# Performance work log

Hardware: AMD Instinct MI355X
Metric: run time of the kernel (lower is better)

Reference implementation:

```python
import jax, jax.numpy as jnp
import numpy as np

NCLASS = 8
THRESH = 0.02
POOL_KS = (32, 16, 8)  # ceil(0.5*64), ceil(0.5*32), ceil(0.5*16)
BN_EPS = 1e-5


def _gcn(x, m, W, b):
    A = m + jnp.eye(x.shape[1], dtype=x.dtype)
    dinv = jax.lax.rsqrt(A.sum(-1))
    An = dinv[:, :, None] * A * dinv[:, None, :]
    return jnp.einsum('bij,bjf->bif', An, x @ W) + b


def _sagpool(x, m, w1, w2, b, k):
    # SAGPooling with GraphConv scorer: s = x w1 + (A x) w2 + b; top-k, gate by tanh
    s = (x @ w1 + jnp.einsum('bij,bjf->bif', m, x) @ w2 + b)[..., 0]
    v, idx = jax.lax.top_k(s, k)
    xg = jnp.take_along_axis(x, idx[:, :, None], axis=1) * jnp.tanh(v)[:, :, None]
    mg = jnp.take_along_axis(jnp.take_along_axis(m, idx[:, :, None], 1), idx[:, None, :], 2)
    return xg, mg


def _readout(x):
    return jnp.concatenate([x.max(1), x.mean(1)], axis=-1)  # [gmp || gep]


def _edist(a, b):
    d2 = (a * a).sum(-1)[:, None] + (b * b).sum(-1)[None, :] - 2.0 * (a @ b.T)
    return jnp.sqrt(jnp.clip(d2, 1e-12))


def _conv1d(x, W, b, dil, pad):
    y = jax.lax.conv_general_dilated(x, W, (1,), [(pad, pad)], rhs_dilation=(dil,),
                                     dimension_numbers=('NCH', 'OIH', 'NCH'))
    return jax.nn.relu(y + b[None, :, None])


def _forward(x, labels, idx_train, gat_W, gat_a1, gat_a2, gcn1_W, gcn1_b, gcn2_W, gcn2_b,
             gcn3_W, gcn3_b, pool1_w1, pool1_w2, pool1_b, pool2_w1, pool2_w2, pool2_b,
             pool3_w1, pool3_w2, pool3_b, gru_Wih, gru_Whh, gru_bih, gru_bhh,
             conv1_W, conv1_b, conv2_W, conv2_b, conv3_W, conv3_b,
             fc0_W, fc0_b, bn0_g, bn0_b, fc1_W, fc1_b, att_W1, att_b1, att_W2, att_b2):
    B, C, L = x.shape
    # GAT-style learned adjacency over the C channel-nodes, thresholded to a sparse graph
    h = x @ gat_W
    e = jax.nn.leaky_relu((h @ gat_a1)[:, :, None] + (h @ gat_a2)[:, None, :], 0.2)
    A = jax.nn.softmax(e, axis=-1)
    m = (A > THRESH).astype(x.dtype)  # [B,C,C] block-diagonal-equivalent mask
    # three GCN + SAGPool stages with summed jump-knowledge readout
    g = jax.nn.relu(_gcn(x, m, gcn1_W, gcn1_b))
    g, m = _sagpool(g, m, pool1_w1, pool1_w2, pool1_b, POOL_KS[0])
    r = _readout(g)
    g = jax.nn.relu(_gcn(g, m, gcn2_W, gcn2_b))
    g, m = _sagpool(g, m, pool2_w1, pool2_w2, pool2_b, POOL_KS[1])
    r = r + _readout(g)
    g = jax.nn.relu(_gcn(g, m, gcn3_W, gcn3_b))
    g, m = _sagpool(g, m, pool3_w1, pool3_w2, pool3_b, POOL_KS[2])
    x_gnn = r + _readout(g)  # [B, 2*hidden]
    # GRU: torch nn.GRU(len_ts, gru_dim) with [N,C,L] -> seq axis 0, batch axis 1 (as in source)
    G = gru_Whh.shape[1]
    def step(hprev, xt):
        gi = xt @ gru_Wih.T + gru_bih
        gh = hprev @ gru_Whh.T + gru_bhh
        ir, iz, inn = jnp.split(gi, 3, axis=-1)
        hr, hz, hn = jnp.split(gh, 3, axis=-1)
        rg = jax.nn.sigmoid(ir + hr)
        zg = jax.nn.sigmoid(iz + hz)
        ng = jnp.tanh(inn + rg * hn)
        hnew = (1.0 - zg) * ng + zg * hprev
        return hnew, hnew
    _, ys = jax.lax.scan(step, jnp.zeros((C, G), x.dtype), x)
    x_gru = ys.mean(1)  # [B, G]
    # dilated conv branch; padding = dilation*(kernel-1) both sides as in __init__
    xc = _conv1d(x, conv1_W, conv1_b, 1, 7)
    xc = _conv1d(xc, conv2_W, conv2_b, 2, 8)
    xc = _conv1d(xc, conv3_W, conv3_b, 4, 8)
    x_conv = xc.mean(2)  # [B, filters[2]]
    feat = jnp.concatenate([x_conv, x_gru, x_gnn], axis=1)
    # mapping MLP: Linear -> BatchNorm(train stats) -> LeakyReLU -> Linear
    hm = feat @ fc0_W + fc0_b
    hm = bn0_g * (hm - hm.mean(0)) * jax.lax.rsqrt(hm.var(0) + BN_EPS) + bn0_b
    hm = jax.nn.leaky_relu(hm, 0.01)
    z = hm @ fc1_W + fc1_b  # [B, 128]
    # per-class attention-weighted prototypes over training samples (masked softmax)
    train = jnp.zeros((B,), bool).at[idx_train].set(True)
    cmask = train[None, :] & (labels[None, :] == jnp.arange(NCLASS)[:, None])
    t = jnp.tanh(jnp.einsum('nd,cda->cna', z, att_W1) + att_b1[:, None, :])
    logits = jnp.einsum('cna,ca->cn', t, att_W2) + att_b2[:, None]
    w = jax.nn.softmax(jnp.where(cmask, logits, -1e30), axis=1)
    proto = w @ z  # [NCLASS, 128]
    pd = jnp.exp(-0.5 * _edist(proto, proto))
    proto_dist = pd.sum() / (NCLASS * (NCLASS - 1) / 2)
    dists = jnp.exp(-0.5 * _edist(z, proto))
    return dists, proto_dist


def setup_inputs() -> dict:
    key = jax.random.key(0)
    ks = iter(jax.random.split(key, 64))
    def rn(shape, s=0.05):
        return jax.random.normal(next(ks), shape, jnp.float32) * s
    B, C, L, H, G, NC, AT, F1 = 256, 64, 512, 128, 128, 8, 64, 128
    inp = {}
    inp['x'] = jax.random.normal(next(ks), (B, C, L), jnp.float32)
    inp['labels'] = jnp.arange(B, dtype=jnp.int32) % NC  # guarantees every class in train split
    inp['idx_train'] = jnp.arange(B // 2, dtype=jnp.int32)
    inp['gat_W'] = rn((L, L)); inp['gat_a1'] = rn((L,)); inp['gat_a2'] = rn((L,))
    inp['gcn1_W'] = rn((L, H)); inp['gcn1_b'] = jnp.zeros((H,), jnp.float32)
    inp['gcn2_W'] = rn((H, H)); inp['gcn2_b'] = jnp.zeros((H,), jnp.float32)
    inp['gcn3_W'] = rn((H, H)); inp['gcn3_b'] = jnp.zeros((H,), jnp.float32)
    for i in (1, 2, 3):
        inp['pool%d_w1' % i] = rn((H, 1)); inp['pool%d_w2' % i] = rn((H, 1))
        inp['pool%d_b' % i] = jnp.zeros((1,), jnp.float32)
    inp['gru_Wih'] = rn((3 * G, L)); inp['gru_Whh'] = rn((3 * G, G))
    inp['gru_bih'] = jnp.zeros((3 * G,), jnp.float32); inp['gru_bhh'] = jnp.zeros((3 * G,), jnp.float32)
    inp['conv1_W'] = rn((F1, C, 8)); inp['conv1_b'] = jnp.zeros((F1,), jnp.float32)
    inp['conv2_W'] = rn((F1, F1, 5)); inp['conv2_b'] = jnp.zeros((F1,), jnp.float32)
    inp['conv3_W'] = rn((F1, F1, 3)); inp['conv3_b'] = jnp.zeros((F1,), jnp.float32)
    inp['fc0_W'] = rn((F1 + G + 2 * H, 256)); inp['fc0_b'] = jnp.zeros((256,), jnp.float32)
    inp['bn0_g'] = jnp.ones((256,), jnp.float32); inp['bn0_b'] = jnp.zeros((256,), jnp.float32)
    inp['fc1_W'] = rn((256, 128)); inp['fc1_b'] = jnp.zeros((128,), jnp.float32)
    inp['att_W1'] = rn((NC, 128, AT)); inp['att_b1'] = jnp.zeros((NC, AT), jnp.float32)
    inp['att_W2'] = rn((NC, AT)); inp['att_b2'] = jnp.zeros((NC,), jnp.float32)
    return inp


def reference(x, labels, idx_train, gat_W, gat_a1, gat_a2, gcn1_W, gcn1_b, gcn2_W, gcn2_b,
              gcn3_W, gcn3_b, pool1_w1, pool1_w2, pool1_b, pool2_w1, pool2_w2, pool2_b,
              pool3_w1, pool3_w2, pool3_b, gru_Wih, gru_Whh, gru_bih, gru_bhh,
              conv1_W, conv1_b, conv2_W, conv2_b, conv3_W, conv3_b,
              fc0_W, fc0_b, bn0_g, bn0_b, fc1_W, fc1_b, att_W1, att_b1, att_W2, att_b2):
    return _forward(x, labels, idx_train, gat_W, gat_a1, gat_a2, gcn1_W, gcn1_b, gcn2_W, gcn2_b,
                    gcn3_W, gcn3_b, pool1_w1, pool1_w2, pool1_b, pool2_w1, pool2_w2, pool2_b,
                    pool3_w1, pool3_w2, pool3_b, gru_Wih, gru_Whh, gru_bih, gru_bhh,
                    conv1_W, conv1_b, conv2_W, conv2_b, conv3_W, conv3_b,
                    fc0_W, fc0_b, bn0_g, bn0_b, fc1_W, fc1_b, att_W1, att_b1, att_W2, att_b2)
```

## Files before the change

kernel.cpp:

```cpp
#include <hip/hip_runtime.h>
#include <math.h>

#define BB 256
#define CC 64
#define LL 512
#define HH 128
#define G3 384
#define NC 8
#define AT 64
#define CL1 519
#define CL2 527
#define CL3 535
#define THRESH 0.02f

typedef _Float16 h2 __attribute__((ext_vector_type(2)));
typedef _Float16 f16x8 __attribute__((ext_vector_type(8)));
typedef float f32x4 __attribute__((ext_vector_type(4)));
union HU { unsigned int u; h2 h; float f; };
union BU { uint4 u; f16x8 h; };

__device__ inline float warp_red_sum(float v) {
  #pragma unroll
  for (int o = 32; o > 0; o >>= 1) v += __shfl_down(v, o, 64);
  return v;
}

__device__ inline float fdot2f(h2 a, h2 b, float c) {
#if __has_builtin(__builtin_amdgcn_fdot2)
  return __builtin_amdgcn_fdot2(a, b, c, false);
#else
  float r;
  asm volatile("v_dot2_f32_f16 %0, %1, %2, %3" : "=v"(r) : "v"(a), "v"(b), "v"(c));
  return r;
#endif
}
__device__ inline h2 asH2(float f) { HU u; u.f = f; return u.h; }
__device__ inline h2 uH2(unsigned int x) { HU u; u.u = x; return u.h; }
__device__ inline unsigned int packh(float a, float b) {
  HU u; h2 t; t.x = (_Float16)a; t.y = (_Float16)b; u.h = t; return u.u;
}
__device__ inline float vexp2(float x) { float r; asm("v_exp_f32 %0, %1" : "=v"(r) : "v"(x)); return r; }
__device__ inline float vrcp(float x)  { float r; asm("v_rcp_f32 %0, %1" : "=v"(r) : "v"(x)); return r; }
__device__ inline float fsigm(float x) { return vrcp(1.f + vexp2(-1.44269504f * x)); }
__device__ inline float ftanh(float x) { return 1.f - 2.f * vrcp(vexp2(2.88539008f * x) + 1.f); }

__device__ inline void packw_one(const float* __restrict__ W, unsigned int* __restrict__ out,
                                 int idx, int cinlog, int KS) {
  int w_ = idx & 3, l = (idx >> 2) & 63, n = (idx >> 8) & 7, c = idx >> 11;
  int CIN = 1 << cinlog;
  int oc = n * 16 + (l & 15);
  int k0 = c * 32 + ((l >> 4) << 3) + 2 * w_;
  int t0 = k0 >> cinlog, ci0 = k0 & (CIN - 1);
  int t1 = (k0 + 1) >> cinlog, ci1 = (k0 + 1) & (CIN - 1);
  out[idx] = packh(W[(size_t)oc * CIN * KS + ci0 * KS + t0],
                   W[(size_t)oc * CIN * KS + ci1 * KS + t1]);
}

__global__ void k_packall(const float* __restrict__ gcnW0, const float* __restrict__ gcnW1,
                          const float* __restrict__ gcnW2, const float* __restrict__ wih,
                          const float* __restrict__ whh,
                          const float* __restrict__ c1W, const float* __restrict__ c2W,
                          const float* __restrict__ c3W,
                          const float* __restrict__ gatW, const float* __restrict__ a1,
                          const float* __restrict__ a2,
                          unsigned int* gw1h, unsigned int* gw2h, unsigned int* gw3h,
                          unsigned int* wihTh, unsigned int* wpk,
                          unsigned int* wt1h, unsigned int* wt2h, unsigned int* wt3h,
                          float* wa1, float* wa2) {
  int idx = blockIdx.x * 256 + threadIdx.x;
  if (idx < 32768) {
    int w_ = idx & 3, l = (idx >> 2) & 63, n = (idx >> 8) & 7, c = idx >> 11;
    int k0 = c * 32 + ((l >> 4) << 3) + 2 * w_;
    int col = n * 16 + (l & 15);
    gw1h[idx] = packh(gcnW0[k0 * 128 + col], gcnW0[(k0 + 1) * 128 + col]);
  } else if (idx < 40960) {
    int t = idx - 32768;
    int w_ = t & 3, l = (t >> 2) & 63, n = (t >> 8) & 7, c = t >> 11;
    int k0 = c * 32 + ((l >> 4) << 3) + 2 * w_;
    int col = n * 16 + (l & 15);
    gw2h[t] = packh(gcnW1[k0 * 128 + col], gcnW1[(k0 + 1) * 128 + col]);
  } else if (idx < 49152) {
    int t = idx - 40960;
    int w_ = t & 3, l = (t >> 2) & 63, n = (t >> 8) & 7, c = t >> 11;
    int k0 = c * 32 + ((l >> 4) << 3) + 2 * w_;
    int col = n * 16 + (l & 15);
    gw3h[t] = packh(gcnW2[k0 * 128 + col], gcnW2[(k0 + 1) * 128 + col]);
  } else if (idx < 147456) {
    int t = idx - 49152;
    int w_ = t & 3, l = (t >> 2) & 63;
    int nfc = t >> 8;
    int n = nfc % 24, c = nfc / 24;
    int k0 = c * 32 + ((l >> 4) << 3) + 2 * w_;
    int col = n * 16 + (l & 15);
    wihTh[t] = packh(wih[col * 512 + k0], wih[col * 512 + k0 + 1]);
  } else if (idx < 172032) {
    int t = idx - 147456; int j = t & 127, rk = t >> 7;
    int r = rk >> 6, k2 = rk & 63;
    const float* src = whh + (size_t)(j + 128 * r) * 128 + 2 * k2;
    wpk[t] = packh(src[0], src[1]);
  } else if (idx < 204800) {
    packw_one(c1W, wt1h, idx - 172032, 6, 8);
  } else if (idx < 245760) {
    packw_one(c2W, wt2h, idx - 204800, 7, 5);
  } else if (idx < 270336) {
    packw_one(c3W, wt3h, idx - 245760, 7, 3);
  } else if (idx < 270848) {
    int l = idx - 270336;
    const float* row = gatW + l * LL;
    float s1 = 0.f, s2 = 0.f;
    for (int k = 0; k < LL; k++) { float w = row[k]; s1 += w * a1[k]; s2 += w * a2[k]; }
    wa1[l] = s1; wa2[l] = s2;
  }
}

__global__ __launch_bounds__(256) void k_gat(const float* __restrict__ x,
                                             const float* __restrict__ wa1,
                                             const float* __restrict__ wa2,
                                             float* __restrict__ mask,
                                             float* __restrict__ dinv) {
  __shared__ float h1s[64], h2s[64];
  int b = blockIdx.x, tid = threadIdx.x;
  int i = tid >> 2, q = tid & 3;
  const float* xr = x + ((size_t)b * 64 + i) * LL + q * 128;
  float s1 = 0.f, s2 = 0.f;
  #pragma unroll 4
  for (int k = 0; k < 128; k += 4) {
    float4 xv = *(const float4*)&xr[k];
    float4 w1 = *(const float4*)&wa1[q * 128 + k];
    float4 w2 = *(const float4*)&wa2[q * 128 + k];
    s1 += xv.x * w1.x + xv.y * w1.y + xv.z * w1.z + xv.w * w1.w;
    s2 += xv.x * w2.x + xv.y * w2.y + xv.z * w2.z + xv.w * w2.w;
  }
  s1 += __shfl_xor(s1, 1, 64); s1 += __shfl_xor(s1, 2, 64);
  s2 += __shfl_xor(s2, 1, 64); s2 += __shfl_xor(s2, 2, 64);
  if (q == 0) { h1s[i] = s1; h2s[i] = s2; }
  __syncthreads();
  float hi = h1s[i];
  float e[16];
  float mx = -3.4e38f;
  #pragma unroll
  for (int u = 0; u < 16; u++) {
    float v = hi + h2s[q * 16 + u];
    v = v < 0.f ? 0.2f * v : v;
    e[u] = v;
    mx = fmaxf(mx, v);
  }
  mx = fmaxf(mx, __shfl_xor(mx, 1, 64));
  mx = fmaxf(mx, __shfl_xor(mx, 2, 64));
  float sm = 0.f;
  #pragma unroll
  for (int u = 0; u < 16; u++) { e[u] = expf(e[u] - mx); sm += e[u]; }
  sm += __shfl_xor(sm, 1, 64); sm += __shfl_xor(sm, 2, 64);
  float cnt = 0.f;
  #pragma unroll
  for (int u = 0; u < 16; u++) {
    float mval = (e[u] / sm > THRESH) ? 1.f : 0.f;
    mask[((size_t)b * 64 + i) * 64 + q * 16 + u] = mval;
    cnt += mval;
  }
  cnt += __shfl_xor(cnt, 1, 64); cnt += __shfl_xor(cnt, 2, 64);
  if (q == 0) dinv[b * 64 + i] = 1.f / sqrtf(cnt + 1.f);
}

__global__ __launch_bounds__(256) void k_gmfma(const float* __restrict__ A,
                                               const uint4* __restrict__ Bf,
                                               void* __restrict__ Cv,
                                               int M, int N, int K, int out16) {
  __shared__ _Float16 as[2][64 * 64];
  int nwg = gridDim.x, bid = blockIdx.x;
  int lb = (bid & 7) * (nwg >> 3) + (bid >> 3);
  int nbn = N >> 7;
  int bm = lb / nbn, bn = lb - bm * nbn;
  int m0 = bm * 64;
  int tid = threadIdx.x, l = tid & 63, w = tid >> 6;
  int NKT = K >> 6, NC2 = K >> 5, N16 = N >> 4;
  int nf0 = bn * 8 + 2 * w, nf1 = nf0 + 1;
  int ar = tid >> 2;
  int ac = (tid & 3) * 16;
  float4 rg[4];
  auto stageA = [&](int kt) {
    const float* src = &A[(size_t)(m0 + ar) * K + kt * 64 + ac];
    rg[0] = *(const float4*)&src[0];
    rg[1] = *(const float4*)&src[4];
    rg[2] = *(const float4*)&src[8];
    rg[3] = *(const float4*)&src[12];
  };
  auto commitA = [&](int buf) {
    int s0 = (tid & 3) * 2;
    int phys0 = (s0 ^ (ar & 7)) * 8;
    int phys1 = ((s0 + 1) ^ (ar & 7)) * 8;
    uint4 v0, v1;
    v0.x = packh(rg[0].x, rg[0].y); v0.y = packh(rg[0].z, rg[0].w);
    v0.z = packh(rg[1].x, rg[1].y); v0.w = packh(rg[1].z, rg[1].w);
    v1.x = packh(rg[2].x, rg[2].y); v1.y = packh(rg[2].z, rg[2].w);
    v1.z = packh(rg[3].x, rg[3].y); v1.w = packh(rg[3].z, rg[3].w);
    *(uint4*)&as[buf][ar * 64 + phys0] = v0;
    *(uint4*)&as[buf][ar * 64 + phys1] = v1;
  };
  f32x4 acc[4][2];
  #pragma unroll
  for (int m = 0; m < 4; m++) {
    acc[m][0] = (f32x4){0.f, 0.f, 0.f, 0.f};
    acc[m][1] = (f32x4){0.f, 0.f, 0.f, 0.f};
  }
  stageA(0); commitA(0);
  uint4 bc0 = Bf[(size_t)nf0 * 64 + l];
  uint4 bc1 = Bf[(size_t)nf1 * 64 + l];
  __syncthreads();
  for (int c = 0; c < NC2; c++) {
    int kt = c >> 1, half = c & 1;
    if (half == 0 && kt + 1 < NKT) stageA(kt + 1);
    uint4 pn0 = bc0, pn1 = bc1;
    if (c + 1 < NC2) {
      pn0 = Bf[(size_t)((c + 1) * N16 + nf0) * 64 + l];
      pn1 = Bf[(size_t)((c + 1) * N16 + nf1) * 64 + l];
    }
    int slotbase = half * 4 + (l >> 4);
    f16x8 a[4];
    #pragma unroll
    for (int m = 0; m < 4; m++) {
      int row = m * 16 + (l & 15);
      int phys = slotbase ^ (row & 7);
      a[m] = *(const f16x8*)&as[kt & 1][row * 64 + phys * 8];
    }
    BU u0, u1; u0.u = bc0; u1.u = bc1;
    #pragma unroll
    for (int m = 0; m < 4; m++) {
      acc[m][0] = __builtin_amdgcn_mfma_f32_16x16x32_f16(a[m], u0.h, acc[m][0], 0, 0, 0);
      acc[m][1] = __builtin_amdgcn_mfma_f32_16x16x32_f16(a[m], u1.h, acc[m][1], 0, 0, 0);
    }
    if (half == 1 && kt + 1 < NKT) {
      commitA((kt + 1) & 1);
      __syncthreads();
    }
    bc0 = pn0; bc1 = pn1;
  }
  if (out16) {
    _Float16* Ch = (_Float16*)Cv;
    #pragma unroll
    for (int n = 0; n < 2; n++) {
      int col = (nf0 + n) * 16 + (l & 15);
      #pragma unroll
      for (int m = 0; m < 4; m++) {
        #pragma unroll
        for (int i = 0; i < 4; i++)
          Ch[(size_t)(m0 + m * 16 + (l >> 4) * 4 + i) * N + col] = (_Float16)acc[m][n][i];
      }
    }
  } else {
    float* Cf = (float*)Cv;
    #pragma unroll
    for (int n = 0; n < 2; n++) {
      int col = (nf0 + n) * 16 + (l & 15);
      #pragma unroll
      for (int m = 0; m < 4; m++) {
        #pragma unroll
        for (int i = 0; i < 4; i++)
          Cf[(size_t)(m0 + m * 16 + (l >> 4) * 4 + i) * N + col] = acc[m][n][i];
      }
    }
  }
}

__global__ void k_gcnagg(const float* __restrict__ xw, const float* __restrict__ mask,
                         const float* __restrict__ dinv, const float* __restrict__ bias,
                         float* __restrict__ gout, int N) {
  __shared__ float mrow[64], dv[64];
  int b = blockIdx.x / N, i = blockIdx.x % N;
  if (threadIdx.x < N) {
    mrow[threadIdx.x] = mask[(size_t)(b * N + i) * N + threadIdx.x];
    dv[threadIdx.x] = dinv[b * N + threadIdx.x];
  }
  __syncthreads();
  int f = threadIdx.x;
  float di = dv[i];
  float acc = di * xw[(size_t)(b * N + i) * HH + f];
  for (int j = 0; j < N; j++) acc += mrow[j] * dv[j] * xw[(size_t)(b * N + j) * HH + f];
  float y = di * acc + bias[f];
  gout[(size_t)(b * N + i) * HH + f] = y > 0.f ? y : 0.f;
}

__global__ __launch_bounds__(256) void k_pool(const float* __restrict__ g,
                                              const float* __restrict__ mask,
                                              const float* __restrict__ w1,
                                              const float* __restrict__ w2,
                                              const float* __restrict__ pb, int N, int kk,
                                              float* gp, float* mnext, float* dnext,
                                              float* __restrict__ r, int accum) {
  __shared__ float gs[64 * 129];
  __shared__ float ms[64 * 65];
  __shared__ float d1s[64], d2s[64], sv[64], vals[32], tvs[32];
  __shared__ int idxs[32];
  int b = blockIdx.x, tid = threadIdx.x;
  for (int q = tid; q < N * 128; q += 256) {
    int row = q >> 7, d = q & 127;
    gs[row * 129 + d] = g[(size_t)(b * N + row) * 128 + d];
  }
  for (int q = tid; q < N * N; q += 256) {
    int row = q / N, u = q - row * N;
    ms[row * 65 + u] = mask[(size_t)(b * N + row) * N + u];
  }
  __syncthreads();
  if (tid < N) {
    float a = 0.f, c = 0.f;
    const float* gr = &gs[tid * 129];
    for (int d = 0; d < 128; d++) { float v = gr[d]; a += v * w1[d]; c += v * w2[d]; }
    d1s[tid] = a; d2s[tid] = c;
  }
  __syncthreads();
  if (tid < N) {
    const float* mr = &ms[tid * 65];
    float s = d1s[tid] + pb[0];
    for (int j = 0; j < N; j++) s += mr[j] * d2s[j];
    sv[tid] = s;
  }
  __syncthreads();
  if (tid < 64) {
    float myv = (tid < N) ? sv[tid] : -3.4e38f;
    int alive = (tid < N) ? 1 : 0;
    for (int t = 0; t < kk; t++) {
      float cv = alive ? myv : -3.4e38f;
      int ci = tid;
      #pragma unroll
      for (int o = 32; o > 0; o >>= 1) {
        float ov = __shfl_xor(cv, o, 64);
        int oi = __shfl_xor(ci, o, 64);
        if (ov > cv || (ov == cv && oi < ci)) { cv = ov; ci = oi; }
      }
      if (tid == ci) alive = 0;
      if (tid == 0) { idxs[t] = ci; vals[t] = cv; }
    }
  }
  __syncthreads();
  if (tid < kk) tvs[tid] = tanhf(vals[tid]);
  __syncthreads();
  if (tid < HH) {
    float mx = -3.4e38f, sm = 0.f;
    for (int t = 0; t < kk; t++) {
      float v = gs[idxs[t] * 129 + tid] * tvs[t];
      if (gp) gp[(size_t)(b * kk + t) * HH + tid] = v;
      mx = fmaxf(mx, v); sm += v;
    }
    float mres = sm / (float)kk;
    if (accum) {
      r[b * 256 + tid] += mx;
      r[b * 256 + 128 + tid] += mres;
    } else {
      r[b * 256 + tid] = mx;
      r[b * 256 + 128 + tid] = mres;
    }
  }
  for (int q = tid; q < kk * kk; q += 256) {
    int t = q / kk, u = q - t * kk;
    mnext[(size_t)(b * kk + t) * kk + u] = ms[idxs[t] * 65 + idxs[u]];
  }
  if (dnext && tid < kk) {
    float s = 0.f;
    for (int u = 0; u < kk; u++) s += ms[idxs[tid] * 65 + idxs[u]];
    dnext[b * kk + tid] = 1.0f / sqrtf(s + 1.0f);
  }
}

__global__ __launch_bounds__(256, 1) void k_gru(const float* __restrict__ gi,
                                                const unsigned int* __restrict__ wpk,
                                                const float* __restrict__ bhh,
                                                const float* __restrict__ bih,
                                                _Float16* __restrict__ ys) {
  __shared__ _Float16 hb[2][128];
  int c = blockIdx.x;
  int j = threadIdx.x >> 1, half = threadIdx.x & 1;
  int kb = half * 32;
  h2 w0[32], w1[32], w2[32];
  #pragma unroll
  for (int kk = 0; kk < 32; kk++) { HU u; u.u = wpk[(kb + kk) * 128 + j]; w0[kk] = u.h; }
  #pragma unroll
  for (int kk = 0; kk < 32; kk++) { HU u; u.u = wpk[(64 + kb + kk) * 128 + j]; w1[kk] = u.h; }
  #pragma unroll
  for (int kk = 0; kk < 32; kk++) { HU u; u.u = wpk[(128 + kb + kk) * 128 + j]; w2[kk] = u.h; }
  float bh0 = bhh[j], bh1 = bhh[j + 128], bh2 = bhh[j + 256];
  float bi0 = bih[j], bi1 = bih[j + 128], bi2 = bih[j + 256];
  float hprev = 0.f;
  if (half == 0) hb[0][j] = (_Float16)0.f;
  __syncthreads();
  const float* gbase = gi + (size_t)c * G3 + j;
  float g0 = gbase[0], g1 = gbase[128], g2 = gbase[256];
  int cur = 0;
  for (int b = 0; b < BB; b++) {
    float n0 = 0.f, n1 = 0.f, n2 = 0.f;
    if (b + 1 < BB) {
      const float* gn = gbase + (size_t)(b + 1) * CC * G3;
      n0 = gn[0]; n1 = gn[128]; n2 = gn[256];
    }
    float a0a = 0.f, a0b = 0.f, a1a = 0.f, a1b = 0.f, a2a = 0.f, a2b = 0.f;
    #pragma unroll
    for (int q = 0; q < 8; q++) {
      float4 hv = *(const float4*)&hb[cur][half * 64 + q * 8];
      h2 h0 = asH2(hv.x), h1 = asH2(hv.y), h2v = asH2(hv.z), h3 = asH2(hv.w);
      a0a = fdot2f(w0[q * 4 + 0], h0, a0a); a0b = fdot2f(w0[q * 4 + 1], h1, a0b);
      a0a = fdot2f(w0[q * 4 + 2], h2v, a0a); a0b = fdot2f(w0[q * 4 + 3], h3, a0b);
      a1a = fdot2f(w1[q * 4 + 0], h0, a1a); a1b = fdot2f(w1[q * 4 + 1], h1, a1b);
      a1a = fdot2f(w1[q * 4 + 2], h2v, a1a); a1b = fdot2f(w1[q * 4 + 3], h3, a1b);
      a2a = fdot2f(w2[q * 4 + 0], h0, a2a); a2b = fdot2f(w2[q * 4 + 1], h1, a2b);
      a2a = fdot2f(w2[q * 4 + 2], h2v, a2a); a2b = fdot2f(w2[q * 4 + 3], h3, a2b);
    }
    float A0 = a0a + a0b, A1 = a1a + a1b, A2 = a2a + a2b;
    A0 += __shfl_xor(A0, 1, 64);
    A1 += __shfl_xor(A1, 1, 64);
    A2 += __shfl_xor(A2, 1, 64);
    A0 += bh0; A1 += bh1; A2 += bh2;
    float rg = fsigm(g0 + bi0 + A0);
    float zg = fsigm(g1 + bi1 + A1);
    float ng = ftanh(g2 + bi2 + rg * A2);
    float hn = (1.f - zg) * ng + zg * hprev;
    hprev = hn;
    if (half == 0) {
      ys[(size_t)(b * CC + c) * 128 + j] = (_Float16)hn;
      hb[cur ^ 1][j] = (_Float16)hn;
    }
    asm volatile("s_waitcnt lgkmcnt(0)" ::: "memory");
    __builtin_amdgcn_s_barrier();
    cur ^= 1;
    g0 = n0; g1 = n1; g2 = n2;
  }
}

template<int CIN, int KS, int DIL, int PAD, int LIN, int LOUT, int MODE>
__global__ __launch_bounds__(256) void k_cmfma(const void* __restrict__ inv,
                                               const uint4* __restrict__ Bf,
                                               const float* __restrict__ bias,
                                               void* __restrict__ outv, int b0) {
  constexpr int QN = CIN / 32;
  constexpr int NCH = KS * QN;
  constexpr int SLOTS = CIN / 8;
  constexpr int NT = (LOUT + 63) / 64;
  __shared__ _Float16 xs[72 * CIN];
  int nb = blockIdx.x / NT;
  int p0 = (blockIdx.x % NT) * 64;
  int tid = threadIdx.x;
  int l = tid & 63, w = tid >> 6;

  if constexpr (MODE == 0) {
    const float* src = (const float*)inv + (size_t)nb * CIN * LIN;
    for (int q = tid; q < (CIN / 2) * 72; q += 256) {
      int ci2 = q / 72, r = q % 72;
      int ci = 2 * ci2;
      int p = p0 - PAD + r;
      float v0 = 0.f, v1 = 0.f;
      if (p >= 0 && p < LIN) { v0 = src[ci * LIN + p]; v1 = src[(ci + 1) * LIN + p]; }
      int slot = ci >> 3;
      int phys = slot ^ (r & 7);
      *(unsigned int*)&xs[r * CIN + phys * 8 + (ci & 7)] = packh(v0, v1);
    }
  } else {
    const _Float16* src = (const _Float16*)inv + (size_t)nb * LIN * CIN;
    for (int q = tid; q < 72 * SLOTS; q += 256) {
      int r = q / SLOTS, s = q % SLOTS;
      int p = p0 - PAD + r;
      uint4 v = make_uint4(0u, 0u, 0u, 0u);
      if (p >= 0 && p < LIN) v = *(const uint4*)&src[(size_t)p * CIN + s * 8];
      int phys = s ^ (r & 7);
      *(uint4*)&xs[r * CIN + phys * 8] = v;
    }
  }
  __syncthreads();

  int n0 = 2 * w, n1 = n0 + 1;
  f32x4 acc[4][2];
  #pragma unroll
  for (int m = 0; m < 4; m++) {
    acc[m][0] = (f32x4){0.f, 0.f, 0.f, 0.f};
    acc[m][1] = (f32x4){0.f, 0.f, 0.f, 0.f};
  }
  uint4 bc0 = Bf[(size_t)(0 * 8 + n0) * 64 + l];
  uint4 bc1 = Bf[(size_t)(0 * 8 + n1) * 64 + l];
  for (int c = 0; c < NCH; c++) {
    uint4 bn0 = bc0, bn1 = bc1;
    if (c + 1 < NCH) {
      bn0 = Bf[(size_t)((c + 1) * 8 + n0) * 64 + l];
      bn1 = Bf[(size_t)((c + 1) * 8 + n1) * 64 + l];
    }
    int t = c / QN, q = c % QN;
    int slotbase = q * 4 + (l >> 4);
    f16x8 a[4];
    #pragma unroll
    for (int m = 0; m < 4; m++) {
      int r = m * 16 + (l & 15) + t * DIL;
      int phys = slotbase ^ (r & 7);
      a[m] = *(const f16x8*)&xs[r * CIN + phys * 8];
    }
    BU u0, u1; u0.u = bc0; u1.u = bc1;
    #pragma unroll
    for (int m = 0; m < 4; m++) {
      acc[m][0] = __builtin_amdgcn_mfma_f32_16x16x32_f16(a[m], u0.h, acc[m][0], 0, 0, 0);
      acc[m][1] = __builtin_amdgcn_mfma_f32_16x16x32_f16(a[m], u1.h, acc[m][1], 0, 0, 0);
    }
    bc0 = bn0; bc1 = bn1;
  }

  if constexpr (MODE == 2) {
    float* xcv = (float*)outv;
    #pragma unroll
    for (int n = 0; n < 2; n++) {
      int oc = (2 * w + n) * 16 + (l & 15);
      float bz = bias[oc];
      float s = 0.f;
      #pragma unroll
      for (int m = 0; m < 4; m++) {
        #pragma unroll
        for (int i = 0; i < 4; i++) {
          int pos = p0 + m * 16 + (l >> 4) * 4 + i;
          if (pos < LOUT) { float y = acc[m][n][i] + bz; s += y > 0.f ? y : 0.f; }
        }
      }
      s += __shfl_xor(s, 16, 64);
      s += __shfl_xor(s, 32, 64);
      if (l < 16) atomicAdd(&xcv[(size_t)(b0 + nb) * 128 + oc], s);
    }
  } else {
    _Float16* outp = (_Float16*)outv + (size_t)nb * LOUT * 128;
    #pragma unroll
    for (int n = 0; n < 2; n++) {
      int oc = (2 * w + n) * 16 + (l & 15);
      float bz = bias[oc];
      #pragma unroll
      for (int m = 0; m < 4; m++) {
        #pragma unroll
        for (int i = 0; i < 4; i++) {
          int pos = p0 + m * 16 + (l >> 4) * 4 + i;
          if (pos < LOUT) {
            float y = acc[m][n][i] + bz;
            outp[(size_t)pos * 128 + oc] = (_Float16)(y > 0.f ? y : 0.f);
          }
        }
      }
    }
  }
}

__global__ void k_fc0(const float* __restrict__ xconv, const _Float16* __restrict__ ys,
                      const float* __restrict__ r, const float* __restrict__ W,
                      const float* __restrict__ bias, float* __restrict__ hm,
                      float* __restrict__ csum, float* __restrict__ csum2) {
  __shared__ float feat[512];
  int b = blockIdx.x, t = threadIdx.x;
  if (t < 128) {
    feat[t] = xconv[b * 128 + t] * (1.f / (float)CL3);
    const _Float16* yb = ys + (size_t)b * CC * 128 + t;
    float acc = 0.f;
    for (int c = 0; c < CC; c++) acc += (float)yb[c * 128];
    feat[128 + t] = acc / 64.f;
  }
  feat[256 + t] = r[b * 256 + t];
  __syncthreads();
  float acc = bias[t];
  for (int k = 0; k < 512; k++) acc += feat[k] * W[k * 256 + t];
  hm[b * 256 + t] = acc;
  atomicAdd(&csum[t], acc);
  atomicAdd(&csum2[t], acc * acc);
}

__global__ void k_fc1bn(const float* __restrict__ hm, const float* __restrict__ csum,
                        const float* __restrict__ csum2, const float* __restrict__ gamma,
                        const float* __restrict__ beta, const float* __restrict__ W,
                        const float* __restrict__ bias, float* __restrict__ z) {
  __shared__ float hs[256];
  int b = blockIdx.x, t = threadIdx.x;
  for (int kk = t; kk < 256; kk += 128) {
    float v = hm[b * 256 + kk];
    float mean = csum[kk] * (1.f / 256.f);
    float var = csum2[kk] * (1.f / 256.f) - mean * mean;
    float y = gamma[kk] * (v - mean) * (1.f / sqrtf(var + 1e-5f)) + beta[kk];
    hs[kk] = y < 0.f ? 0.01f * y : y;
  }
  __syncthreads();
  float acc = bias[t];
  for (int k = 0; k < 256; k++) acc += hs[k] * W[k * 128 + t];
  z[b * 128 + t] = acc;
}

__global__ __launch_bounds__(256) void k_att1(const float* __restrict__ z,
                                              const float* __restrict__ W1,
                                              const float* __restrict__ b1,
                                              const float* __restrict__ W2,
                                              float* __restrict__ logits) {
  __shared__ float sa[32][64];
  __shared__ float sb[32][64];
  int c = blockIdx.x >> 2;
  int m0 = (blockIdx.x & 3) * 64;
  const float* B = W1 + (size_t)c * 128 * AT;
  int tx = threadIdx.x & 15, ty = threadIdx.x >> 4;
  float acc[4][4];
  #pragma unroll
  for (int i = 0; i < 4; i++)
    #pragma unroll
    for (int j = 0; j < 4; j++) acc[i][j] = 0.f;
  int arow = threadIdx.x >> 2;
  int acol = (threadIdx.x & 3) * 8;
  int brow = threadIdx.x >> 4;
  int bcol = (threadIdx.x & 15) * 4;
  for (int k0 = 0; k0 < 128; k0 += 32) {
    float4 av0 = *(const float4*)&z[(size_t)(m0 + arow) * 128 + k0 + acol];
    float4 av1 = *(const float4*)&z[(size_t)(m0 + arow) * 128 + k0 + acol + 4];
    float4 bv0 = *(const float4*)&B[(size_t)(k0 + brow) * AT + bcol];
    float4 bv1 = *(const float4*)&B[(size_t)(k0 + brow + 16) * AT + bcol];
    __syncthreads();
    sa[acol + 0][arow] = av0.x; sa[acol + 1][arow] = av0.y;
    sa[acol + 2][arow] = av0.z; sa[acol + 3][arow] = av0.w;
    sa[acol + 4][arow] = av1.x; sa[acol + 5][arow] = av1.y;
    sa[acol + 6][arow] = av1.z; sa[acol + 7][arow] = av1.w;
    *(float4*)&sb[brow][bcol] = bv0;
    *(float4*)&sb[brow + 16][bcol] = bv1;
    __syncthreads();
    #pragma unroll
    for (int kk = 0; kk < 32; kk++) {
      float4 a4 = *(const float4*)&sa[kk][ty * 4];
      float4 b4 = *(const float4*)&sb[kk][tx * 4];
      acc[0][0] += a4.x * b4.x; acc[0][1] += a4.x * b4.y; acc[0][2] += a4.x * b4.z; acc[0][3] += a4.x * b4.w;
      acc[1][0] += a4.y * b4.x; acc[1][1] += a4.y * b4.y; acc[1][2] += a4.y * b4.z; acc[1][3] += a4.y * b4.w;
      acc[2][0] += a4.z * b4.x; acc[2][1] += a4.z * b4.y; acc[2][2] += a4.z * b4.z; acc[2][3] += a4.z * b4.w;
      acc[3][0] += a4.w * b4.x; acc[3][1] += a4.w * b4.y; acc[3][2] += a4.w * b4.z; acc[3][3] += a4.w * b4.w;
    }
  }
  const float* b1c = b1 + c * AT;
  const float* w2c = W2 + c * AT;
  float w2v[4], b1v[4];
  #pragma unroll
  for (int j = 0; j < 4; j++) { w2v[j] = w2c[tx * 4 + j]; b1v[j] = b1c[tx * 4 + j]; }
  #pragma unroll
  for (int i = 0; i < 4; i++) {
    float s = 0.f;
    #pragma unroll
    for (int j = 0; j < 4; j++) s += tanhf(acc[i][j] + b1v[j]) * w2v[j];
    #pragma unroll
    for (int o = 8; o > 0; o >>= 1) s += __shfl_xor(s, o, 64);
    if (tx == 0) logits[c * 256 + m0 + ty * 4 + i] = s;
  }
}

__global__ void k_att2(const float* __restrict__ z, const int* __restrict__ labels,
                       const int* __restrict__ idx_train, int ntrain,
                       const float* __restrict__ logits, const float* __restrict__ b2,
                       float* __restrict__ protos) {
  __shared__ float wv[256], red[256];
  __shared__ int trainm[256];
  int c = blockIdx.x, n = threadIdx.x;
  trainm[n] = 0; __syncthreads();
  if (n < ntrain) trainm[idx_train[n]] = 1;
  __syncthreads();
  bool keep = trainm[n] && (labels[n] == c);
  float ml = keep ? (logits[c * 256 + n] + b2[c]) : -1e30f;
  red[n] = ml; __syncthreads();
  for (int s = 128; s > 0; s >>= 1) { if (n < s) red[n] = fmaxf(red[n], red[n + s]); __syncthreads(); }
  float mx = red[0]; __syncthreads();
  float e = expf(ml - mx);
  wv[n] = e; red[n] = e; __syncthreads();
  for (int s = 128; s > 0; s >>= 1) { if (n < s) red[n] += red[n + s]; __syncthreads(); }
  float ssum = red[0]; __syncthreads();
  wv[n] = wv[n] / ssum;
  __syncthreads();
  if (n < 128) {
    float p = 0.f;
    for (int q = 0; q < 256; q++) p += wv[q] * z[q * 128 + n];
    protos[c * 128 + n] = p;
  }
}

__global__ void k_dist(const float* __restrict__ z, const float* __restrict__ protos,
                       float* __restrict__ dout) {
  if (blockIdx.x == BB) {
    int t = threadIdx.x;
    if (t < 64) {
      int i = t >> 3, jx = t & 7;
      float dot = 0.f, p2i = 0.f, p2j = 0.f;
      for (int d = 0; d < 128; d++) {
        float a = protos[i * 128 + d], bb2 = protos[jx * 128 + d];
        dot += a * bb2; p2i += a * a; p2j += bb2 * bb2;
      }
      float d2 = fmaxf(p2i + p2j - 2.f * dot, 1e-12f);
      float e = expf(-0.5f * sqrtf(d2));
      e = warp_red_sum(e);
      if (t == 0) dout[2048] = e / 28.f;
    }
    return;
  }
  __shared__ float zs[128], red[128];
  int n = blockIdx.x, t = threadIdx.x;
  zs[t] = z[n * 128 + t];
  red[t] = zs[t] * zs[t]; __syncthreads();
  for (int s = 64; s > 0; s >>= 1) { if (t < s) red[t] += red[t + s]; __syncthreads(); }
  float z2 = red[0];
  if (t < NC) {
    float dot = 0.f, p2 = 0.f;
    const float* pr = protos + t * 128;
    for (int d = 0; d < 128; d++) { float pv = pr[d]; dot += pv * zs[d]; p2 += pv * pv; }
    float d2 = fmaxf(z2 + p2 - 2.f * dot, 1e-12f);
    dout[n * NC + t] = expf(-0.5f * sqrtf(d2));
  }
}

extern "C" void kernel_launch(void* const* d_in, const int* in_sizes, int n_in,
                              void* d_out, int out_size, void* d_ws, size_t ws_size,
                              hipStream_t stream) {
  const float* x = (const float*)d_in[0];
  const int* labels = (const int*)d_in[1];
  const int* idx_train = (const int*)d_in[2];
  const float* gat_W = (const float*)d_in[3];
  const float* gat_a1 = (const float*)d_in[4];
  const float* gat_a2 = (const float*)d_in[5];
  const float* gcnW[3] = {(const float*)d_in[6], (const float*)d_in[8], (const float*)d_in[10]};
  const float* gcnB[3] = {(const float*)d_in[7], (const float*)d_in[9], (const float*)d_in[11]};
  const float* pw1[3] = {(const float*)d_in[12], (const float*)d_in[15], (const float*)d_in[18]};
  const float* pw2[3] = {(const float*)d_in[13], (const float*)d_in[16], (const float*)d_in[19]};
  const float* pbb[3] = {(const float*)d_in[14], (const float*)d_in[17], (const float*)d_in[20]};
  const float* wih = (const float*)d_in[21];
  const float* whh = (const float*)d_in[22];
  const float* bih = (const float*)d_in[23];
  const float* bhh = (const float*)d_in[24];
  const float* c1W = (const float*)d_in[25]; const float* c1b = (const float*)d_in[26];
  const float* c2W = (const float*)d_in[27]; const float* c2b = (const float*)d_in[28];
  const float* c3W = (const float*)d_in[29]; const float* c3b = (const float*)d_in[30];
  const float* fc0W = (const float*)d_in[31]; const float* fc0b = (const float*)d_in[32];
  const float* bn0g = (const float*)d_in[33]; const float* bn0b = (const float*)d_in[34];
  const float* fc1W = (const float*)d_in[35]; const float* fc1b = (const float*)d_in[36];
  const float* aW1 = (const float*)d_in[37]; const float* ab1 = (const float*)d_in[38];
  const float* aW2 = (const float*)d_in[39]; const float* ab2 = (const float*)d_in[40];
  float* out = (float*)d_out;
  float* ws = (float*)d_ws;

  size_t off = 0;
  auto take = [&](size_t n) { size_t o = off; off += (n + 63) & ~(size_t)63; return o; };
  float* wa1   = ws + take(512);
  float* wa2   = ws + take(512);
  float* dinv  = ws + take(BB * 64);
  float* rbuf  = ws + take(BB * 256);
  float* xconv = ws + take(BB * 128);
  float* csum  = ws + take(256);
  float* csum2 = ws + take(256);
  float* hm    = ws + take(BB * 256);
  float* zb    = ws + take(BB * 128);
  float* protos = ws + take(NC * 128);
  float* lgts  = ws + take(NC * 256);
  float* ysf   = ws + take(1048576);
  float* gw1h  = ws + take(256 * 128);
  float* gw2h  = ws + take(64 * 128);
  float* gw3h  = ws + take(64 * 128);
  float* wpkf  = ws + take(192 * 128);
  float* wihThf = ws + take(98304);
  float* wtcf  = ws + take(98304);
  float* Z     = ws + take(8568832);
  float* mA  = Z;
  float* mB  = Z + 1048576;
  float* xw  = Z + 2097152;
  float* gb  = Z + 4194304;
  float* gp1 = Z + 6291456;
  float* gp2 = Z + 7340032;
  float* gi = Z;
  float* cv1 = Z;
  float* cv2 = Z + 4251648;
  _Float16* ysh = (_Float16*)ysf;
  unsigned int* wpk = (unsigned int*)wpkf;
  unsigned int* wihTh = (unsigned int*)wihThf;
  unsigned int* wt1h = (unsigned int*)wtcf;
  unsigned int* wt2h = wt1h + 32768;
  unsigned int* wt3h = wt2h + 40960;

  hipMemsetAsync(xconv, 0, (BB * 128 + 512) * sizeof(float), stream);

  k_packall<<<1058, 256, 0, stream>>>(gcnW[0], gcnW[1], gcnW[2], wih, whh,
                                      c1W, c2W, c3W, gat_W, gat_a1, gat_a2,
                                      (unsigned int*)gw1h, (unsigned int*)gw2h,
                                      (unsigned int*)gw3h, wihTh, wpk,
                                      wt1h, wt2h, wt3h, wa1, wa2);

  k_gat<<<BB, 256, 0, stream>>>(x, wa1, wa2, mA, dinv);

  const int Ns[3] = {64, 32, 16};
  const int ks[3] = {32, 16, 8};
  const int Kin[3] = {512, 128, 128};
  const float* gins[3] = {x, gp1, gp2};
  const unsigned int* gwh[3] = {(unsigned int*)gw1h, (unsigned int*)gw2h, (unsigned int*)gw3h};
  float* mcur[3] = {mA, mB, mA};
  float* mnxt[3] = {mB, mA, mB};
  float* gps[3]  = {gp1, gp2, nullptr};
  for (int s = 0; s < 3; s++) {
    int N = Ns[s];
    k_gmfma<<<(BB * N / 64), 256, 0, stream>>>(
        gins[s], (const uint4*)gwh[s], xw, BB * N, HH, Kin[s], 0);
    k_gcnagg<<<BB * N, 128, 0, stream>>>(xw, mcur[s], dinv, gcnB[s], gb, N);
    k_pool<<<BB, 256, 0, stream>>>(gb, mcur[s], pw1[s], pw2[s], pbb[s], N, ks[s],
                                   gps[s], mnxt[s], s < 2 ? dinv : nullptr, rbuf, s);
  }

  k_gmfma<<<(BB * CC / 64) * 3, 256, 0, stream>>>(
      x, (const uint4*)wihTh, gi, BB * CC, G3, LL, 0);
  k_gru<<<CC, 256, 0, stream>>>(gi, wpk, bhh, bih, ysh);

  for (int bc = 0; bc < 2; bc++) {
    int b0 = bc * 128;
    k_cmfma<64, 8, 1, 7, 512, CL1, 0><<<128 * 9, 256, 0, stream>>>(
        x + (size_t)b0 * CC * LL, (const uint4*)wt1h, c1b, cv1, b0);
    k_cmfma<128, 5, 2, 8, CL1, CL2, 1><<<128 * 9, 256, 0, stream>>>(
        cv1, (const uint4*)wt2h, c2b, cv2, b0);
    k_cmfma<128, 3, 4, 8, CL2, CL3, 2><<<128 * 9, 256, 0, stream>>>(
        cv2, (const uint4*)wt3h, c3b, xconv, b0);
  }

  k_fc0<<<BB, 256, 0, stream>>>(xconv, ysh, rbuf, fc0W, fc0b, hm, csum, csum2);
  k_fc1bn<<<BB, 128, 0, stream>>>(hm, csum, csum2, bn0g, bn0b, fc1W, fc1b, zb);
  k_att1<<<NC * 4, 256, 0, stream>>>(zb, aW1, ab1, aW2, lgts);
  k_att2<<<NC, 256, 0, stream>>>(zb, labels, idx_train, in_sizes[2], lgts, ab2, protos);
  k_dist<<<BB + 1, 128, 0, stream>>>(zb, protos, out);
}
```

Baseline: 484.9 us.

## Fuse GCN aggregation into pooling, store GRU gates in fp16, unchunk conv batches

Merges the per-row GCN aggregation kernel into a templated pooling kernel. Each block now aggregates a whole graph in shared memory and scores, top-k selects and gathers it without writing the intermediate to global memory. The GRU input projection is stored and read as fp16, which halves its memory traffic at some cost in precision. The conv stack runs over the full batch in one launch per layer using dedicated workspace buffers instead of two half-batch chunks, so there are fewer launches but a larger workspace footprint.

```diff
diff --git a/kernel.cpp b/kernel.cpp
--- a/kernel.cpp
+++ b/kernel.cpp
@@ -262,50 +262,116 @@
   }
 }
 
-__global__ void k_gcnagg(const float* __restrict__ xw, const float* __restrict__ mask,
-                         const float* __restrict__ dinv, const float* __restrict__ bias,
-                         float* __restrict__ gout, int N) {
-  __shared__ float mrow[64], dv[64];
-  int b = blockIdx.x / N, i = blockIdx.x % N;
-  if (threadIdx.x < N) {
-    mrow[threadIdx.x] = mask[(size_t)(b * N + i) * N + threadIdx.x];
-    dv[threadIdx.x] = dinv[b * N + threadIdx.x];
-  }
-  __syncthreads();
-  int f = threadIdx.x;
-  float di = dv[i];
-  float acc = di * xw[(size_t)(b * N + i) * HH + f];
-  for (int j = 0; j < N; j++) acc += mrow[j] * dv[j] * xw[(size_t)(b * N + j) * HH + f];
-  float y = di * acc + bias[f];
-  gout[(size_t)(b * N + i) * HH + f] = y > 0.f ? y : 0.f;
-}
-
-__global__ __launch_bounds__(256) void k_pool(const float* __restrict__ g,
-                                              const float* __restrict__ mask,
-                                              const float* __restrict__ w1,
-                                              const float* __restrict__ w2,
-                                              const float* __restrict__ pb, int N, int kk,
-                                              float* gp, float* mnext, float* dnext,
-                                              float* __restrict__ r, int accum) {
-  __shared__ float gs[64 * 129];
-  __shared__ float ms[64 * 65];
+template<int N, int KK>
+__global__ __launch_bounds__(256) void k_gcnpool(const float* __restrict__ xw,
+                                                 const float* __restrict__ mask,
+                                                 const float* __restrict__ dinv,
+                                                 const float* __restrict__ bias,
+                                                 const float* __restrict__ w1,
+                                                 const float* __restrict__ w2,
+                                                 const float* __restrict__ pb,
+                                                 float* gp, float* mnext, float* dnext,
+                                                 float* __restrict__ r, int accum) {
+  constexpr int RPT = (N >= 32) ? (N / 32) : 1;
+  constexpr int NRG = N / RPT;
+  __shared__ float xs[N * 132];
+  __shared__ float ms[N * 65];
+  __shared__ float dv[64];
   __shared__ float d1s[64], d2s[64], sv[64], vals[32], tvs[32];
   __shared__ int idxs[32];
   int b = blockIdx.x, tid = threadIdx.x;
-  for (int q = tid; q < N * 128; q += 256) {
-    int row = q >> 7, d = q & 127;
-    gs[row * 129 + d] = g[(size_t)(b * N + row) * 128 + d];
+  for (int q = tid; q < N * 32; q += 256) {
+    int i = q >> 5, fo = (q & 31) * 4;
+    *(float4*)&xs[i * 132 + fo] = *(const float4*)&xw[((size_t)b * N + i) * 128 + fo];
   }
   for (int q = tid; q < N * N; q += 256) {
     int row = q / N, u = q - row * N;
     ms[row * 65 + u] = mask[(size_t)(b * N + row) * N + u];
   }
-  __syncthreads();
-  if (tid < N) {
-    float a = 0.f, c = 0.f;
-    const float* gr = &gs[tid * 129];
-    for (int d = 0; d < 128; d++) { float v = gr[d]; a += v * w1[d]; c += v * w2[d]; }
-    d1s[tid] = a; d2s[tid] = c;
+  if (tid < N) dv[tid] = dinv[b * N + tid];
+  __syncthreads();
+  for (int q = tid; q < N * 32; q += 256) {
+    int i = q >> 5, fo = (q & 31) * 4;
+    float4 v = *(float4*)&xs[i * 132 + fo];
+    float d = dv[i];
+    v.x *= d; v.y *= d; v.z *= d; v.w *= d;
+    *(float4*)&xs[i * 132 + fo] = v;
+  }
+  __syncthreads();
+  int ri = tid >> 3, fq = tid & 7, f0 = fq * 16;
+  float g[RPT][16];
+  if (ri < NRG) {
+    float acc[RPT][16];
+    #pragma unroll
+    for (int p = 0; p < RPT; p++)
+      #pragma unroll
+      for (int e = 0; e < 16; e++) acc[p][e] = 0.f;
+    for (int j = 0; j < N; j++) {
+      float4 xa = *(const float4*)&xs[j * 132 + f0];
+      float4 xb = *(const float4*)&xs[j * 132 + f0 + 4];
+      float4 xc = *(const float4*)&xs[j * 132 + f0 + 8];
+      float4 xd = *(const float4*)&xs[j * 132 + f0 + 12];
+      #pragma unroll
+      for (int p = 0; p < RPT; p++) {
+        float m = ms[(ri * RPT + p) * 65 + j];
+        acc[p][0] += m * xa.x;  acc[p][1] += m * xa.y;
+        acc[p][2] += m * xa.z;  acc[p][3] += m * xa.w;
+        acc[p][4] += m * xb.x;  acc[p][5] += m * xb.y;
+        acc[p][6] += m * xb.z;  acc[p][7] += m * xb.w;
+        acc[p][8] += m * xc.x;  acc[p][9] += m * xc.y;
+        acc[p][10] += m * xc.z; acc[p][11] += m * xc.w;
+        acc[p][12] += m * xd.x; acc[p][13] += m * xd.y;
+        acc[p][14] += m * xd.z; acc[p][15] += m * xd.w;
+      }
+    }
+    float bz[16];
+    #pragma unroll
+    for (int e = 0; e < 16; e++) bz[e] = bias[f0 + e];
+    #pragma unroll
+    for (int p = 0; p < RPT; p++) {
+      int i = ri * RPT + p;
+      float di = dv[i];
+      float4 sa = *(const float4*)&xs[i * 132 + f0];
+      float4 sb = *(const float4*)&xs[i * 132 + f0 + 4];
+      float4 sc = *(const float4*)&xs[i * 132 + f0 + 8];
+      float4 sd = *(const float4*)&xs[i * 132 + f0 + 12];
+      float sx[16] = {sa.x, sa.y, sa.z, sa.w, sb.x, sb.y, sb.z, sb.w,
+                      sc.x, sc.y, sc.z, sc.w, sd.x, sd.y, sd.z, sd.w};
+      #pragma unroll
+      for (int e = 0; e < 16; e++) {
+        float y = di * (sx[e] + acc[p][e]) + bz[e];
+        g[p][e] = y > 0.f ? y : 0.f;
+      }
+    }
+  }
+  __syncthreads();
+  if (ri < NRG) {
+    #pragma unroll
+    for (int p = 0; p < RPT; p++) {
+      int i = ri * RPT + p;
+      float4 va = {g[p][0], g[p][1], g[p][2], g[p][3]};
+      float4 vb = {g[p][4], g[p][5], g[p][6], g[p][7]};
+      float4 vc = {g[p][8], g[p][9], g[p][10], g[p][11]};
+      float4 vd = {g[p][12], g[p][13], g[p][14], g[p][15]};
+      *(float4*)&xs[i * 132 + f0] = va;
+      *(float4*)&xs[i * 132 + f0 + 4] = vb;
+      *(float4*)&xs[i * 132 + f0 + 8] = vc;
+      *(float4*)&xs[i * 132 + f0 + 12] = vd;
+    }
+  }
+  __syncthreads();
+  {
+    int i = tid >> 2, q4 = tid & 3;
+    if (i < N) {
+      float a = 0.f, c = 0.f;
+      const float* gr = &xs[i * 132 + q4 * 32];
+      const float* w1p = &w1[q4 * 32];
+      const float* w2p = &w2[q4 * 32];
+      for (int d = 0; d < 32; d++) { float v = gr[d]; a += v * w1p[d]; c += v * w2p[d]; }
+      a += __shfl_xor(a, 1, 64); a += __shfl_xor(a, 2, 64);
+      c += __shfl_xor(c, 1, 64); c += __shfl_xor(c, 2, 64);
+      if (q4 == 0) { d1s[i] = a; d2s[i] = c; }
+    }
   }
   __syncthreads();
   if (tid < N) {
@@ -318,7 +384,7 @@
   if (tid < 64) {
     float myv = (tid < N) ? sv[tid] : -3.4e38f;
     int alive = (tid < N) ? 1 : 0;
-    for (int t = 0; t < kk; t++) {
+    for (int t = 0; t < KK; t++) {
       float cv = alive ? myv : -3.4e38f;
       int ci = tid;
       #pragma unroll
@@ -332,16 +398,16 @@
     }
   }
   __syncthreads();
-  if (tid < kk) tvs[tid] = tanhf(vals[tid]);
+  if (tid < KK) tvs[tid] = tanhf(vals[tid]);
   __syncthreads();
   if (tid < HH) {
     float mx = -3.4e38f, sm = 0.f;
-    for (int t = 0; t < kk; t++) {
-      float v = gs[idxs[t] * 129 + tid] * tvs[t];
-      if (gp) gp[(size_t)(b * kk + t) * HH + tid] = v;
+    for (int t = 0; t < KK; t++) {
+      float v = xs[idxs[t] * 132 + tid] * tvs[t];
+      if (gp) gp[(size_t)(b * KK + t) * HH + tid] = v;
       mx = fmaxf(mx, v); sm += v;
     }
-    float mres = sm / (float)kk;
+    float mres = sm / (float)KK;
     if (accum) {
       r[b * 256 + tid] += mx;
       r[b * 256 + 128 + tid] += mres;
@@ -350,18 +416,18 @@
       r[b * 256 + 128 + tid] = mres;
     }
   }
-  for (int q = tid; q < kk * kk; q += 256) {
-    int t = q / kk, u = q - t * kk;
-    mnext[(size_t)(b * kk + t) * kk + u] = ms[idxs[t] * 65 + idxs[u]];
-  }
-  if (dnext && tid < kk) {
+  for (int q = tid; q < KK * KK; q += 256) {
+    int t = q / KK, u = q - t * KK;
+    mnext[(size_t)(b * KK + t) * KK + u] = ms[idxs[t] * 65 + idxs[u]];
+  }
+  if (dnext && tid < KK) {
     float s = 0.f;
-    for (int u = 0; u < kk; u++) s += ms[idxs[tid] * 65 + idxs[u]];
-    dnext[b * kk + tid] = 1.0f / sqrtf(s + 1.0f);
-  }
-}
-
-__global__ __launch_bounds__(256, 1) void k_gru(const float* __restrict__ gi,
+    for (int u = 0; u < KK; u++) s += ms[idxs[tid] * 65 + idxs[u]];
+    dnext[b * KK + tid] = 1.0f / sqrtf(s + 1.0f);
+  }
+}
+
+__global__ __launch_bounds__(256, 1) void k_gru(const _Float16* __restrict__ gi,
                                                 const unsigned int* __restrict__ wpk,
                                                 const float* __restrict__ bhh,
                                                 const float* __restrict__ bih,
@@ -382,14 +448,14 @@
   float hprev = 0.f;
   if (half == 0) hb[0][j] = (_Float16)0.f;
   __syncthreads();
-  const float* gbase = gi + (size_t)c * G3 + j;
-  float g0 = gbase[0], g1 = gbase[128], g2 = gbase[256];
+  const _Float16* gbase = gi + (size_t)c * G3 + j;
+  float g0 = (float)gbase[0], g1 = (float)gbase[128], g2 = (float)gbase[256];
   int cur = 0;
   for (int b = 0; b < BB; b++) {
     float n0 = 0.f, n1 = 0.f, n2 = 0.f;
     if (b + 1 < BB) {
-      const float* gn = gbase + (size_t)(b + 1) * CC * G3;
-      n0 = gn[0]; n1 = gn[128]; n2 = gn[256];
+      const _Float16* gn = gbase + (size_t)(b + 1) * CC * G3;
+      n0 = (float)gn[0]; n1 = (float)gn[128]; n2 = (float)gn[256];
     }
     float a0a = 0.f, a0b = 0.f, a1a = 0.f, a1b = 0.f, a2a = 0.f, a2b = 0.f;
     #pragma unroll
@@ -747,16 +813,15 @@
   float* wpkf  = ws + take(192 * 128);
   float* wihThf = ws + take(98304);
   float* wtcf  = ws + take(98304);
+  float* cv1f  = ws + take(8503296);
+  float* cv2f  = ws + take(8634368);
   float* Z     = ws + take(8568832);
   float* mA  = Z;
   float* mB  = Z + 1048576;
   float* xw  = Z + 2097152;
-  float* gb  = Z + 4194304;
   float* gp1 = Z + 6291456;
   float* gp2 = Z + 7340032;
-  float* gi = Z;
-  float* cv1 = Z;
-  float* cv2 = Z + 4251648;
+  _Float16* gih = (_Float16*)Z;
   _Float16* ysh = (_Float16*)ysf;
   unsigned int* wpk = (unsigned int*)wpkf;
   unsigned int* wihTh = (unsigned int*)wihThf;
@@ -774,36 +839,26 @@
 
   k_gat<<<BB, 256, 0, stream>>>(x, wa1, wa2, mA, dinv);
 
-  const int Ns[3] = {64, 32, 16};
-  const int ks[3] = {32, 16, 8};
-  const int Kin[3] = {512, 128, 128};
-  const float* gins[3] = {x, gp1, gp2};
-  const unsigned int* gwh[3] = {(unsigned int*)gw1h, (unsigned int*)gw2h, (unsigned int*)gw3h};
-  float* mcur[3] = {mA, mB, mA};
-  float* mnxt[3] = {mB, mA, mB};
-  float* gps[3]  = {gp1, gp2, nullptr};
-  for (int s = 0; s < 3; s++) {
-    int N = Ns[s];
-    k_gmfma<<<(BB * N / 64), 256, 0, stream>>>(
-        gins[s], (const uint4*)gwh[s], xw, BB * N, HH, Kin[s], 0);
-    k_gcnagg<<<BB * N, 128, 0, stream>>>(xw, mcur[s], dinv, gcnB[s], gb, N);
-    k_pool<<<BB, 256, 0, stream>>>(gb, mcur[s], pw1[s], pw2[s], pbb[s], N, ks[s],
-                                   gps[s], mnxt[s], s < 2 ? dinv : nullptr, rbuf, s);
-  }
+  k_gmfma<<<BB * 64 / 64, 256, 0, stream>>>(x, (const uint4*)gw1h, xw, BB * 64, HH, 512, 0);
+  k_gcnpool<64, 32><<<BB, 256, 0, stream>>>(xw, mA, dinv, gcnB[0], pw1[0], pw2[0], pbb[0],
+                                            gp1, mB, dinv, rbuf, 0);
+  k_gmfma<<<BB * 32 / 64, 256, 0, stream>>>(gp1, (const uint4*)gw2h, xw, BB * 32, HH, 128, 0);
+  k_gcnpool<32, 16><<<BB, 256, 0, stream>>>(xw, mB, dinv, gcnB[1], pw1[1], pw2[1], pbb[1],
+                                            gp2, mA, dinv, rbuf, 1);
+  k_gmfma<<<BB * 16 / 64, 256, 0, stream>>>(gp2, (const uint4*)gw3h, xw, BB * 16, HH, 128, 0);
+  k_gcnpool<16, 8><<<BB, 256, 0, stream>>>(xw, mA, dinv, gcnB[2], pw1[2], pw2[2], pbb[2],
+                                           nullptr, mB, nullptr, rbuf, 1);
 
   k_gmfma<<<(BB * CC / 64) * 3, 256, 0, stream>>>(
-      x, (const uint4*)wihTh, gi, BB * CC, G3, LL, 0);
-  k_gru<<<CC, 256, 0, stream>>>(gi, wpk, bhh, bih, ysh);
-
-  for (int bc = 0; bc < 2; bc++) {
-    int b0 = bc * 128;
-    k_cmfma<64, 8, 1, 7, 512, CL1, 0><<<128 * 9, 256, 0, stream>>>(
-        x + (size_t)b0 * CC * LL, (const uint4*)wt1h, c1b, cv1, b0);
-    k_cmfma<128, 5, 2, 8, CL1, CL2, 1><<<128 * 9, 256, 0, stream>>>(
-        cv1, (const uint4*)wt2h, c2b, cv2, b0);
-    k_cmfma<128, 3, 4, 8, CL2, CL3, 2><<<128 * 9, 256, 0, stream>>>(
-        cv2, (const uint4*)wt3h, c3b, xconv, b0);
-  }
+      x, (const uint4*)wihTh, gih, BB * CC, G3, LL, 1);
+  k_gru<<<CC, 256, 0, stream>>>(gih, wpk, bhh, bih, ysh);
+
+  k_cmfma<64, 8, 1, 7, 512, CL1, 0><<<BB * 9, 256, 0, stream>>>(
+      x, (const uint4*)wt1h, c1b, cv1f, 0);
+  k_cmfma<128, 5, 2, 8, CL1, CL2, 1><<<BB * 9, 256, 0, stream>>>(
+      cv1f, (const uint4*)wt2h, c2b, cv2f, 0);
+  k_cmfma<128, 3, 4, 8, CL2, CL3, 2><<<BB * 9, 256, 0, stream>>>(
+      cv2f, (const uint4*)wt3h, c3b, xconv, 0);
 
   k_fc0<<<BB, 256, 0, stream>>>(xconv, ysh, rbuf, fc0W, fc0b, hm, csum, csum2);
   k_fc1bn<<<BB, 128, 0, stream>>>(hm, csum, csum2, bn0g, bn0b, fc1W, fc1b, zb);
```

Measured after the change: 509.9 us. 5.2% more time.
